# Optimization experiments

Measured on AMD Instinct MI355X. Metric: run time of the kernel, lower is better.

Reference implementation:

```python
import jax, jax.numpy as jnp
import numpy as np

B, DIM, T, H = 8, 1024, 2048, 16
HD = DIM // H  # per-head channel dim = 64


def _toeplitz(v):
    # v: (H, T) -> (H, T, T) with M[h, i, j] = v[h, j - i] if j >= i else 0
    m = v.shape[-1]
    i = jnp.arange(m)[:, None]
    j = jnp.arange(m)[None, :]
    idx = jnp.where(j >= i, j - i, 0)
    return jnp.where(j >= i, v[..., idx], jnp.zeros((), v.dtype))


def setup_inputs() -> dict:
    key = jax.random.key(0)
    ks = jax.random.split(key, 5)
    s = 1.0 / np.sqrt(DIM)
    return {
        "x": jax.random.normal(ks[0], (B, DIM, T), jnp.float32),
        "w_in": jax.random.normal(ks[1], (DIM, DIM), jnp.float32) * s,
        "b_in": jnp.zeros((DIM,), jnp.float32),
        "w_out": jax.random.normal(ks[2], (DIM, DIM), jnp.float32) * s,
        "b_out": jnp.zeros((DIM,), jnp.float32),
        "toep_w": jax.random.normal(ks[3], (H, T), jnp.float32) * 0.02,
        "toep_b": jnp.zeros((H, T), jnp.float32),
    }


def reference(x, w_in, b_in, w_out, b_out, toep_w, toep_b):
    # x: (B, DIM, T) -> (B, T, DIM)
    xt = jnp.transpose(x, (0, 2, 1))
    h1 = xt @ w_in.T + b_in  # (B, T, DIM)
    # (B, T, H*HD) -> (B, H, HD, T)
    p = jnp.transpose(h1.reshape(B, T, H, HD), (0, 2, 3, 1))
    M = _toeplitz(toep_w)  # (H, T, T)
    # bmm with per-head causal Toeplitz matrix + per-head bias over time
    conv = jnp.einsum("bhdt,htu->bhdu", p, M) + toep_b[None, :, None, :]
    # (B, H, HD, T) -> (B, T, H*HD)
    merged = jnp.transpose(conv, (0, 3, 1, 2)).reshape(B, T, DIM)
    out = merged @ w_out.T + b_out  # (B, T, DIM)
    return jnp.transpose(out, (0, 2, 1))  # (B, DIM, T)
```

## Files before the change

### kernel.cpp

```cpp
#include <hip/hip_runtime.h>
#include <hip/hip_bf16.h>
#include <stdint.h>

#define B_   8
#define DIM  1024
#define T_   2048
#define H_   16
#define HD   64

typedef __attribute__((ext_vector_type(8))) short bf16x8;
typedef __attribute__((ext_vector_type(4))) float f32x4;

__device__ __forceinline__ unsigned short f2bf(float f) {
    union { float f; unsigned u; } v{f};
    unsigned r = v.u + 0x7fffu + ((v.u >> 16) & 1u);
    return (unsigned short)(r >> 16);
}

__device__ __forceinline__ void gl_lds16(const unsigned short* g, unsigned short* l) {
    __builtin_amdgcn_global_load_lds(
        (const __attribute__((address_space(1))) void*)(const void*)g,
        (__attribute__((address_space(3))) void*)(void*)l,
        16, 0, 0);
}

__device__ __forceinline__ bf16x8 ld_frag(const unsigned short* smem, int row, int cg) {
    return *reinterpret_cast<const bf16x8*>(smem + row * 64 + (((cg) ^ (row & 7)) << 3));
}

__global__ void xpose_cast(const float* __restrict__ x, unsigned short* __restrict__ xt) {
    __shared__ float tile[64][65];
    const int b = blockIdx.z;
    const int d0 = blockIdx.y * 64, t0 = blockIdx.x * 64;
    const int tid = threadIdx.x;
    const int c = tid & 63;
    const int r0 = tid >> 6;

    const float* xp = x + ((size_t)b * DIM + d0) * T_ + t0;
#pragma unroll
    for (int i = 0; i < 16; ++i) {
        int r = r0 + i * 4;
        tile[r][c] = xp[(size_t)r * T_ + c];
    }
    __syncthreads();
    unsigned short* op = xt + ((size_t)b * T_ + t0) * DIM + d0;
#pragma unroll
    for (int i = 0; i < 16; ++i) {
        int r = r0 + i * 4;
        op[(size_t)r * DIM + c] = f2bf(tile[c][r]);
    }
}

__global__ void cast_weights(const float* __restrict__ w_in, const float* __restrict__ w_out,
                             const float* __restrict__ tw,
                             unsigned short* __restrict__ w_in_b, unsigned short* __restrict__ w_out_b,
                             unsigned short* __restrict__ tw_b) {
    int i = blockIdx.x * 256 + threadIdx.x;
    if (i < DIM * DIM) {
        w_in_b[i]  = f2bf(w_in[i]);
        w_out_b[i] = f2bf(w_out[i]);
    }
    if (i < H_ * T_) tw_b[i] = f2bf(tw[i]);
}

__global__ void gen_mfrag(const unsigned short* __restrict__ twb, unsigned short* __restrict__ Mf) {
    const int h = blockIdx.y, dg = blockIdx.x;
    const int D = (dg - 1) * 64;
    unsigned short* out = Mf + (((size_t)h * 32 + dg) << 13);
    for (int v = threadIdx.x; v < 1024; v += 256) {
        int cg = v >> 7, row = v & 127;
        bf16x8 w;
#pragma unroll
        for (int j = 0; j < 8; ++j) {
            int lag = D + row - (cg * 8 + j);
            w[j] = (lag >= 0) ? (short)twb[h * T_ + lag] : (short)0;
        }
        *reinterpret_cast<bf16x8*>(out + (size_t)v * 8) = w;
    }
}

template <bool OUT_BF16>
__global__ void gemm_k(const unsigned short* __restrict__ Aw,
                       const unsigned short* __restrict__ Bm,
                       const float* __restrict__ bias,
                       void* __restrict__ Out) {
    __shared__ __align__(16) unsigned short As[128 * 64];
    __shared__ __align__(16) unsigned short Bs[128 * 64];

    const int flat = blockIdx.x;
    const int wid  = (flat & 7) * 128 + (flat >> 3);
    const int nx   = wid & 15;
    const int my   = (wid >> 4) & 7;
    const int b    = wid >> 7;

    const int tid = threadIdx.x, lane = tid & 63, wv = tid >> 6;
    const int m0 = my * 128;
    const int n0 = nx * 128;
    const unsigned short* Bb = Bm + (size_t)b * T_ * DIM;

    const int wr = wv >> 1, wc = wv & 1;
    const int lrow = lane & 15, lg = lane >> 4;

    f32x4 acc[4][4] = {};

    for (int k0 = 0; k0 < DIM; k0 += 64) {
        __syncthreads();
#pragma unroll
        for (int it = 0; it < 4; ++it) {
            int ch = wv * 4 + it;
            int r  = ch * 8 + (lane >> 3);
            int g  = (lane & 7) ^ (lane >> 3);
            gl_lds16(Aw + (size_t)(m0 + r) * DIM + k0 + g * 8, As + ch * 512);
            gl_lds16(Bb + (size_t)(n0 + r) * DIM + k0 + g * 8, Bs + ch * 512);
        }
        __syncthreads();

#pragma unroll
        for (int kk = 0; kk < 2; ++kk) {
            bf16x8 af[4], bfr[4];
#pragma unroll
            for (int mt = 0; mt < 4; ++mt) af[mt]  = ld_frag(As, wr * 64 + mt * 16 + lrow, kk * 4 + lg);
#pragma unroll
            for (int nt = 0; nt < 4; ++nt) bfr[nt] = ld_frag(Bs, wc * 64 + nt * 16 + lrow, kk * 4 + lg);
#pragma unroll
            for (int mt = 0; mt < 4; ++mt)
#pragma unroll
                for (int nt = 0; nt < 4; ++nt)
                    acc[mt][nt] = __builtin_amdgcn_mfma_f32_16x16x32_bf16(af[mt], bfr[nt], acc[mt][nt], 0, 0, 0);
        }
    }

    const size_t ob = (size_t)b * DIM * T_;
#pragma unroll
    for (int mt = 0; mt < 4; ++mt) {
        int d = m0 + wr * 64 + mt * 16 + lg * 4;
#pragma unroll
        for (int nt = 0; nt < 4; ++nt) {
            int t = n0 + wc * 64 + nt * 16 + lrow;
#pragma unroll
            for (int r = 0; r < 4; ++r) {
                float v = acc[mt][nt][r] + bias[d + r];
                if constexpr (OUT_BF16)
                    ((unsigned short*)Out)[ob + (size_t)(d + r) * T_ + t] = f2bf(v);
                else
                    ((float*)Out)[ob + (size_t)(d + r) * T_ + t] = v;
            }
        }
    }
}

__global__ void conv4_k(const unsigned short* __restrict__ H1,
                        const unsigned short* __restrict__ Mf,
                        const float* __restrict__ tb,
                        unsigned short* __restrict__ Cb) {
    __shared__ __align__(16) unsigned short Ps[2][64 * 64];

    const int flat = blockIdx.x;
    const int wid  = (flat & 7) * 128 + (flat >> 3);
    const int bx   = wid & 7;
    const int b    = (wid >> 3) & 7;
    const int h    = wid >> 6;

    const int tid = threadIdx.x, lane = tid & 63, wv = tid >> 6;
    const unsigned short* Hb = H1 + ((size_t)b * DIM + h * HD) * T_;
    const unsigned short* Ah = Mf + ((size_t)h * 32) * 8192;

    const int lrow = lane & 15, lg = lane >> 4;
    const int rsub = lane >> 3;
    const int g = (lane & 7) ^ rsub;

    const int aoff = (lg * 128 + wv * 32 + lrow) * 8;

#pragma unroll
    for (int ph = 0; ph < 2; ++ph) {
        const int ut = ph ? bx : (T_ / 128 - 1 - bx);
        const int u0 = ut * 128;
        const int nk = 2 * ut + 2;
        f32x4 acc[2][4] = {};

#pragma unroll
        for (int it = 0; it < 2; ++it) {
            int ch = wv * 2 + it;
            int r  = ch * 8 + rsub;
            gl_lds16(Hb + (size_t)r * T_ + g * 8, &Ps[0][0] + ch * 512);
        }
        __syncthreads();

        for (int kt = 0; kt < nk; ++kt) {
            const int cur = kt & 1;
            if (kt + 1 < nk) {
                const int t0n = (kt + 1) * 64;
#pragma unroll
                for (int it = 0; it < 2; ++it) {
                    int ch = wv * 2 + it;
                    int r  = ch * 8 + rsub;
                    gl_lds16(Hb + (size_t)r * T_ + t0n + g * 8, &Ps[cur ^ 1][0] + ch * 512);
                }
            }
            const int dg = 2 * ut - kt + 1;
            const unsigned short* At = Ah + (size_t)dg * 8192;
            bf16x8 af0[2], af1[2];
#pragma unroll
            for (int mt = 0; mt < 2; ++mt) {
                af0[mt] = *reinterpret_cast<const bf16x8*>(At + aoff + mt * 128);
                af1[mt] = *reinterpret_cast<const bf16x8*>(At + 4096 + aoff + mt * 128);
            }
            const unsigned short* Pb = &Ps[cur][0];
            bf16x8 bfr[4];
#pragma unroll
            for (int nt = 0; nt < 4; ++nt) bfr[nt] = ld_frag(Pb, nt * 16 + lrow, lg);
#pragma unroll
            for (int mt = 0; mt < 2; ++mt)
#pragma unroll
                for (int nt = 0; nt < 4; ++nt)
                    acc[mt][nt] = __builtin_amdgcn_mfma_f32_16x16x32_bf16(af0[mt], bfr[nt], acc[mt][nt], 0, 0, 0);
#pragma unroll
            for (int nt = 0; nt < 4; ++nt) bfr[nt] = ld_frag(Pb, nt * 16 + lrow, 4 + lg);
#pragma unroll
            for (int mt = 0; mt < 2; ++mt)
#pragma unroll
                for (int nt = 0; nt < 4; ++nt)
                    acc[mt][nt] = __builtin_amdgcn_mfma_f32_16x16x32_bf16(af1[mt], bfr[nt], acc[mt][nt], 0, 0, 0);

            __syncthreads();
        }

        const size_t base = (size_t)b * T_ * DIM + (size_t)h * HD;
#pragma unroll
        for (int mt = 0; mt < 2; ++mt) {
            int u = u0 + wv * 32 + mt * 16 + lg * 4;
            const float* tbp = tb + h * T_ + u;
            float t0v = tbp[0], t1v = tbp[1], t2v = tbp[2], t3v = tbp[3];
#pragma unroll
            for (int nt = 0; nt < 4; ++nt) {
                int d = nt * 16 + lrow;
                size_t p = base + (size_t)u * DIM + d;
                Cb[p]           = f2bf(acc[mt][nt][0] + t0v);
                Cb[p + DIM]     = f2bf(acc[mt][nt][1] + t1v);
                Cb[p + 2 * DIM] = f2bf(acc[mt][nt][2] + t2v);
                Cb[p + 3 * DIM] = f2bf(acc[mt][nt][3] + t3v);
            }
        }
    }
}

extern "C" void kernel_launch(void* const* d_in, const int* in_sizes, int n_in,
                              void* d_out, int out_size, void* d_ws, size_t ws_size,
                              hipStream_t stream) {
    (void)in_sizes; (void)n_in; (void)out_size; (void)ws_size;
    const float* x      = (const float*)d_in[0];
    const float* w_in   = (const float*)d_in[1];
    const float* b_in   = (const float*)d_in[2];
    const float* w_out  = (const float*)d_in[3];
    const float* b_out  = (const float*)d_in[4];
    const float* toep_w = (const float*)d_in[5];
    const float* toep_b = (const float*)d_in[6];

    char* ws = (char*)d_ws;
    unsigned short* XT    = (unsigned short*)(ws);
    unsigned short* H1    = (unsigned short*)(ws + 33554432);
    unsigned short* Cbuf  = (unsigned short*)(ws + 67108864);
    unsigned short* winb  = (unsigned short*)(ws + 100663296);
    unsigned short* woutb = (unsigned short*)(ws + 102760448);
    unsigned short* twb   = (unsigned short*)(ws + 104857600);
    unsigned short* Mfrag = (unsigned short*)(ws + 104923136);

    xpose_cast<<<dim3(T_ / 64, DIM / 64, B_), dim3(256), 0, stream>>>(x, XT);
    cast_weights<<<dim3((DIM * DIM) / 256), dim3(256), 0, stream>>>(w_in, w_out, toep_w, winb, woutb, twb);
    gen_mfrag<<<dim3(32, H_), dim3(256), 0, stream>>>(twb, Mfrag);
    gemm_k<true><<<dim3(1024), dim3(256), 0, stream>>>(winb, XT, b_in, (void*)H1);
    conv4_k<<<dim3(1024), dim3(256), 0, stream>>>(H1, Mfrag, toep_b, Cbuf);
    gemm_k<false><<<dim3(1024), dim3(256), 0, stream>>>(woutb, Cbuf, b_out, d_out);
}
```

Measured before the change: 145.3 us.

## Double-buffer GEMM and conv LDS tiles with prefetch depth two

Both the projection GEMM and the Toeplitz conv kernel now keep two LDS stages in flight. They prefetch tiles two iterations ahead using explicit vmcnt waits and raw s_barrier instead of __syncthreads. Fragments are read into registers before the buffer is refilled, and the MFMA block runs at raised wave priority. The goal is to hide global-to-LDS latency behind matrix math. The cost is doubled LDS in the GEMM (64KB), which may cut occupancy, and fragile hand-tuned waitcnt logic.

```diff
diff --git a/kernel.cpp b/kernel.cpp
--- a/kernel.cpp
+++ b/kernel.cpp
@@ -84,8 +84,8 @@
                        const unsigned short* __restrict__ Bm,
                        const float* __restrict__ bias,
                        void* __restrict__ Out) {
-    __shared__ __align__(16) unsigned short As[128 * 64];
-    __shared__ __align__(16) unsigned short Bs[128 * 64];
+    __shared__ __align__(16) unsigned short As[2][128 * 64];
+    __shared__ __align__(16) unsigned short Bs[2][128 * 64];
 
     const int flat = blockIdx.x;
     const int wid  = (flat & 7) * 128 + (flat >> 3);
@@ -100,34 +100,62 @@
 
     const int wr = wv >> 1, wc = wv & 1;
     const int lrow = lane & 15, lg = lane >> 4;
+    const int rsub = lane >> 3;
+    const int g = (lane & 7) ^ rsub;
 
     f32x4 acc[4][4] = {};
 
-    for (int k0 = 0; k0 < DIM; k0 += 64) {
-        __syncthreads();
+    auto STAGE = [&](int kt, int p) {
+        const int k0 = kt * 64;
 #pragma unroll
         for (int it = 0; it < 4; ++it) {
             int ch = wv * 4 + it;
-            int r  = ch * 8 + (lane >> 3);
-            int g  = (lane & 7) ^ (lane >> 3);
-            gl_lds16(Aw + (size_t)(m0 + r) * DIM + k0 + g * 8, As + ch * 512);
-            gl_lds16(Bb + (size_t)(n0 + r) * DIM + k0 + g * 8, Bs + ch * 512);
-        }
-        __syncthreads();
-
-#pragma unroll
-        for (int kk = 0; kk < 2; ++kk) {
-            bf16x8 af[4], bfr[4];
-#pragma unroll
-            for (int mt = 0; mt < 4; ++mt) af[mt]  = ld_frag(As, wr * 64 + mt * 16 + lrow, kk * 4 + lg);
-#pragma unroll
-            for (int nt = 0; nt < 4; ++nt) bfr[nt] = ld_frag(Bs, wc * 64 + nt * 16 + lrow, kk * 4 + lg);
-#pragma unroll
-            for (int mt = 0; mt < 4; ++mt)
-#pragma unroll
-                for (int nt = 0; nt < 4; ++nt)
-                    acc[mt][nt] = __builtin_amdgcn_mfma_f32_16x16x32_bf16(af[mt], bfr[nt], acc[mt][nt], 0, 0, 0);
-        }
+            int r  = ch * 8 + rsub;
+            gl_lds16(Aw + (size_t)(m0 + r) * DIM + k0 + g * 8, &As[p][0] + ch * 512);
+            gl_lds16(Bb + (size_t)(n0 + r) * DIM + k0 + g * 8, &Bs[p][0] + ch * 512);
+        }
+    };
+
+    STAGE(0, 0);
+    STAGE(1, 1);
+
+    const int NT = DIM / 64;
+    for (int i = 0; i < NT; ++i) {
+        const int cur = i & 1;
+        if (i + 1 < NT) asm volatile("s_waitcnt vmcnt(8)" ::: "memory");
+        else            asm volatile("s_waitcnt vmcnt(0)" ::: "memory");
+        __builtin_amdgcn_s_barrier();
+        __builtin_amdgcn_sched_barrier(0);
+
+        const unsigned short* Ab = &As[cur][0];
+        const unsigned short* Bf = &Bs[cur][0];
+        bf16x8 a0[4], b0[4], a1[4], b1[4];
+#pragma unroll
+        for (int mt = 0; mt < 4; ++mt) a0[mt] = ld_frag(Ab, wr * 64 + mt * 16 + lrow, lg);
+#pragma unroll
+        for (int nt = 0; nt < 4; ++nt) b0[nt] = ld_frag(Bf, wc * 64 + nt * 16 + lrow, lg);
+#pragma unroll
+        for (int mt = 0; mt < 4; ++mt) a1[mt] = ld_frag(Ab, wr * 64 + mt * 16 + lrow, 4 + lg);
+#pragma unroll
+        for (int nt = 0; nt < 4; ++nt) b1[nt] = ld_frag(Bf, wc * 64 + nt * 16 + lrow, 4 + lg);
+
+        asm volatile("s_waitcnt lgkmcnt(0)" ::: "memory");
+        __builtin_amdgcn_s_barrier();
+        __builtin_amdgcn_sched_barrier(0);
+        if (i + 2 < NT) STAGE(i + 2, cur);
+
+        __builtin_amdgcn_s_setprio(1);
+#pragma unroll
+        for (int mt = 0; mt < 4; ++mt)
+#pragma unroll
+            for (int nt = 0; nt < 4; ++nt)
+                acc[mt][nt] = __builtin_amdgcn_mfma_f32_16x16x32_bf16(a0[mt], b0[nt], acc[mt][nt], 0, 0, 0);
+#pragma unroll
+        for (int mt = 0; mt < 4; ++mt)
+#pragma unroll
+            for (int nt = 0; nt < 4; ++nt)
+                acc[mt][nt] = __builtin_amdgcn_mfma_f32_16x16x32_bf16(a1[mt], b1[nt], acc[mt][nt], 0, 0, 0);
+        __builtin_amdgcn_s_setprio(0);
     }
 
     const size_t ob = (size_t)b * DIM * T_;
@@ -149,7 +177,7 @@
     }
 }
 
-__global__ void conv4_k(const unsigned short* __restrict__ H1,
+__global__ void conv5_k(const unsigned short* __restrict__ H1,
                         const unsigned short* __restrict__ Mf,
                         const float* __restrict__ tb,
                         unsigned short* __restrict__ Cb) {
@@ -171,6 +199,16 @@
 
     const int aoff = (lg * 128 + wv * 32 + lrow) * 8;
 
+    auto PSTAGE = [&](int kt, int p) {
+        const int t0 = kt * 64;
+#pragma unroll
+        for (int it = 0; it < 2; ++it) {
+            int ch = wv * 2 + it;
+            int r  = ch * 8 + rsub;
+            gl_lds16(Hb + (size_t)r * T_ + t0 + g * 8, &Ps[p][0] + ch * 512);
+        }
+    };
+
 #pragma unroll
     for (int ph = 0; ph < 2; ++ph) {
         const int ut = ph ? bx : (T_ / 128 - 1 - bx);
@@ -178,25 +216,23 @@
         const int nk = 2 * ut + 2;
         f32x4 acc[2][4] = {};
 
-#pragma unroll
-        for (int it = 0; it < 2; ++it) {
-            int ch = wv * 2 + it;
-            int r  = ch * 8 + rsub;
-            gl_lds16(Hb + (size_t)r * T_ + g * 8, &Ps[0][0] + ch * 512);
-        }
-        __syncthreads();
+        PSTAGE(0, 0);
+        PSTAGE(1, 1);
 
         for (int kt = 0; kt < nk; ++kt) {
             const int cur = kt & 1;
-            if (kt + 1 < nk) {
-                const int t0n = (kt + 1) * 64;
-#pragma unroll
-                for (int it = 0; it < 2; ++it) {
-                    int ch = wv * 2 + it;
-                    int r  = ch * 8 + rsub;
-                    gl_lds16(Hb + (size_t)r * T_ + t0n + g * 8, &Ps[cur ^ 1][0] + ch * 512);
-                }
-            }
+            if (kt + 1 < nk) asm volatile("s_waitcnt vmcnt(2)" ::: "memory");
+            else             asm volatile("s_waitcnt vmcnt(0)" ::: "memory");
+            __builtin_amdgcn_s_barrier();
+            __builtin_amdgcn_sched_barrier(0);
+
+            const unsigned short* Pb = &Ps[cur][0];
+            bf16x8 p0[4], p1[4];
+#pragma unroll
+            for (int nt = 0; nt < 4; ++nt) p0[nt] = ld_frag(Pb, nt * 16 + lrow, lg);
+#pragma unroll
+            for (int nt = 0; nt < 4; ++nt) p1[nt] = ld_frag(Pb, nt * 16 + lrow, 4 + lg);
+
             const int dg = 2 * ut - kt + 1;
             const unsigned short* At = Ah + (size_t)dg * 8192;
             bf16x8 af0[2], af1[2];
@@ -205,24 +241,24 @@
                 af0[mt] = *reinterpret_cast<const bf16x8*>(At + aoff + mt * 128);
                 af1[mt] = *reinterpret_cast<const bf16x8*>(At + 4096 + aoff + mt * 128);
             }
-            const unsigned short* Pb = &Ps[cur][0];
-            bf16x8 bfr[4];
-#pragma unroll
-            for (int nt = 0; nt < 4; ++nt) bfr[nt] = ld_frag(Pb, nt * 16 + lrow, lg);
+
+            asm volatile("s_waitcnt lgkmcnt(0)" ::: "memory");
+            __builtin_amdgcn_s_barrier();
+            __builtin_amdgcn_sched_barrier(0);
+            if (kt + 2 < nk) PSTAGE(kt + 2, cur);
+
+            __builtin_amdgcn_s_setprio(1);
 #pragma unroll
             for (int mt = 0; mt < 2; ++mt)
 #pragma unroll
                 for (int nt = 0; nt < 4; ++nt)
-                    acc[mt][nt] = __builtin_amdgcn_mfma_f32_16x16x32_bf16(af0[mt], bfr[nt], acc[mt][nt], 0, 0, 0);
-#pragma unroll
-            for (int nt = 0; nt < 4; ++nt) bfr[nt] = ld_frag(Pb, nt * 16 + lrow, 4 + lg);
+                    acc[mt][nt] = __builtin_amdgcn_mfma_f32_16x16x32_bf16(af0[mt], p0[nt], acc[mt][nt], 0, 0, 0);
 #pragma unroll
             for (int mt = 0; mt < 2; ++mt)
 #pragma unroll
                 for (int nt = 0; nt < 4; ++nt)
-                    acc[mt][nt] = __builtin_amdgcn_mfma_f32_16x16x32_bf16(af1[mt], bfr[nt], acc[mt][nt], 0, 0, 0);
-
-            __syncthreads();
+                    acc[mt][nt] = __builtin_amdgcn_mfma_f32_16x16x32_bf16(af1[mt], p1[nt], acc[mt][nt], 0, 0, 0);
+            __builtin_amdgcn_s_setprio(0);
         }
 
         const size_t base = (size_t)b * T_ * DIM + (size_t)h * HD;
@@ -269,6 +305,6 @@
     cast_weights<<<dim3((DIM * DIM) / 256), dim3(256), 0, stream>>>(w_in, w_out, toep_w, winb, woutb, twb);
     gen_mfrag<<<dim3(32, H_), dim3(256), 0, stream>>>(twb, Mfrag);
     gemm_k<true><<<dim3(1024), dim3(256), 0, stream>>>(winb, XT, b_in, (void*)H1);
-    conv4_k<<<dim3(1024), dim3(256), 0, stream>>>(H1, Mfrag, toep_b, Cbuf);
+    conv5_k<<<dim3(1024), dim3(256), 0, stream>>>(H1, Mfrag, toep_b, Cbuf);
     gemm_k<false><<<dim3(1024), dim3(256), 0, stream>>>(woutb, Cbuf, b_out, d_out);
 }
```

After: 319.5 us. 120% more time.

## Double-buffer GEMM LDS tiles and vectorize transpose-cast stores

Applied to the files above, without the earlier changes.

The projection GEMM kernel now keeps two LDS buffers for the A and B tiles. It issues the global-to-LDS load for the next K tile before computing on the current one, with a single barrier per iteration, so load latency can overlap the MFMAs. The transpose-cast kernel also writes four bf16 values per thread as one 8-byte store instead of scalar 2-byte stores. Doubling the GEMM's LDS footprint to 64 KB may reduce occupancy.

```diff
diff --git a/kernel.cpp b/kernel.cpp
--- a/kernel.cpp
+++ b/kernel.cpp
@@ -10,6 +10,7 @@
 
 typedef __attribute__((ext_vector_type(8))) short bf16x8;
 typedef __attribute__((ext_vector_type(4))) float f32x4;
+typedef __attribute__((ext_vector_type(4))) unsigned short u16x4;
 
 __device__ __forceinline__ unsigned short f2bf(float f) {
     union { float f; unsigned u; } v{f};
@@ -44,10 +45,15 @@
     }
     __syncthreads();
     unsigned short* op = xt + ((size_t)b * T_ + t0) * DIM + d0;
-#pragma unroll
-    for (int i = 0; i < 16; ++i) {
-        int r = r0 + i * 4;
-        op[(size_t)r * DIM + c] = f2bf(tile[c][r]);
+    const int ci = (tid & 15) * 4;
+    const int rr = tid >> 4;
+#pragma unroll
+    for (int i = 0; i < 4; ++i) {
+        int r = rr + i * 16;
+        u16x4 v;
+#pragma unroll
+        for (int j = 0; j < 4; ++j) v[j] = f2bf(tile[ci + j][r]);
+        *reinterpret_cast<u16x4*>(op + (size_t)r * DIM + ci) = v;
     }
 }
 
@@ -84,8 +90,8 @@
                        const unsigned short* __restrict__ Bm,
                        const float* __restrict__ bias,
                        void* __restrict__ Out) {
-    __shared__ __align__(16) unsigned short As[128 * 64];
-    __shared__ __align__(16) unsigned short Bs[128 * 64];
+    __shared__ __align__(16) unsigned short As[2][128 * 64];
+    __shared__ __align__(16) unsigned short Bs[2][128 * 64];
 
     const int flat = blockIdx.x;
     const int wid  = (flat & 7) * 128 + (flat >> 3);
@@ -100,34 +106,46 @@
 
     const int wr = wv >> 1, wc = wv & 1;
     const int lrow = lane & 15, lg = lane >> 4;
+    const int rsub = lane >> 3;
+    const int g = (lane & 7) ^ rsub;
 
     f32x4 acc[4][4] = {};
 
-    for (int k0 = 0; k0 < DIM; k0 += 64) {
-        __syncthreads();
+    auto STAGE = [&](int kt, int p) {
+        const int k0 = kt * 64;
 #pragma unroll
         for (int it = 0; it < 4; ++it) {
             int ch = wv * 4 + it;
-            int r  = ch * 8 + (lane >> 3);
-            int g  = (lane & 7) ^ (lane >> 3);
-            gl_lds16(Aw + (size_t)(m0 + r) * DIM + k0 + g * 8, As + ch * 512);
-            gl_lds16(Bb + (size_t)(n0 + r) * DIM + k0 + g * 8, Bs + ch * 512);
-        }
-        __syncthreads();
-
+            int r  = ch * 8 + rsub;
+            gl_lds16(Aw + (size_t)(m0 + r) * DIM + k0 + g * 8, &As[p][0] + ch * 512);
+            gl_lds16(Bb + (size_t)(n0 + r) * DIM + k0 + g * 8, &Bs[p][0] + ch * 512);
+        }
+    };
+
+    STAGE(0, 0);
+    __syncthreads();
+
+    const int NT = DIM / 64;
+    for (int i = 0; i < NT; ++i) {
+        const int cur = i & 1;
+        if (i + 1 < NT) STAGE(i + 1, cur ^ 1);
+
+        const unsigned short* Ab = &As[cur][0];
+        const unsigned short* Bf = &Bs[cur][0];
 #pragma unroll
         for (int kk = 0; kk < 2; ++kk) {
             bf16x8 af[4], bfr[4];
 #pragma unroll
-            for (int mt = 0; mt < 4; ++mt) af[mt]  = ld_frag(As, wr * 64 + mt * 16 + lrow, kk * 4 + lg);
-#pragma unroll
-            for (int nt = 0; nt < 4; ++nt) bfr[nt] = ld_frag(Bs, wc * 64 + nt * 16 + lrow, kk * 4 + lg);
+            for (int mt = 0; mt < 4; ++mt) af[mt]  = ld_frag(Ab, wr * 64 + mt * 16 + lrow, kk * 4 + lg);
+#pragma unroll
+            for (int nt = 0; nt < 4; ++nt) bfr[nt] = ld_frag(Bf, wc * 64 + nt * 16 + lrow, kk * 4 + lg);
 #pragma unroll
             for (int mt = 0; mt < 4; ++mt)
 #pragma unroll
                 for (int nt = 0; nt < 4; ++nt)
                     acc[mt][nt] = __builtin_amdgcn_mfma_f32_16x16x32_bf16(af[mt], bfr[nt], acc[mt][nt], 0, 0, 0);
         }
+        __syncthreads();
     }
 
     const size_t ob = (size_t)b * DIM * T_;
```

Result: slower. 155.1 us (+6.8%).

## Process two batches per conv block, vectorize transpose stores, fuse toeplitz cast

Applied to the files above, without the earlier changes.

The Toeplitz conv kernel now handles two batch elements per workgroup, so each Toeplitz matrix fragment loaded from global memory feeds twice as many MFMAs. The grid is halved and per-wave accumulators double. Separately, the transpose-cast kernel writes four bf16 values per store instead of one, and the toeplitz weight cast is folded into fragment generation, which removes one buffer. The extra accumulator registers and the halved grid (512 blocks) may reduce occupancy.

```diff
diff --git a/kernel.cpp b/kernel.cpp
--- a/kernel.cpp
+++ b/kernel.cpp
@@ -10,6 +10,7 @@
 
 typedef __attribute__((ext_vector_type(8))) short bf16x8;
 typedef __attribute__((ext_vector_type(4))) float f32x4;
+typedef __attribute__((ext_vector_type(4))) unsigned short u16x4;
 
 __device__ __forceinline__ unsigned short f2bf(float f) {
     union { float f; unsigned u; } v{f};
@@ -44,28 +45,31 @@
     }
     __syncthreads();
     unsigned short* op = xt + ((size_t)b * T_ + t0) * DIM + d0;
-#pragma unroll
-    for (int i = 0; i < 16; ++i) {
-        int r = r0 + i * 4;
-        op[(size_t)r * DIM + c] = f2bf(tile[c][r]);
+    const int ci = (tid & 15) * 4;
+    const int rr = tid >> 4;
+#pragma unroll
+    for (int i = 0; i < 4; ++i) {
+        int r = rr + i * 16;
+        u16x4 v;
+#pragma unroll
+        for (int j = 0; j < 4; ++j) v[j] = f2bf(tile[ci + j][r]);
+        *reinterpret_cast<u16x4*>(op + (size_t)r * DIM + ci) = v;
     }
 }
 
 __global__ void cast_weights(const float* __restrict__ w_in, const float* __restrict__ w_out,
-                             const float* __restrict__ tw,
-                             unsigned short* __restrict__ w_in_b, unsigned short* __restrict__ w_out_b,
-                             unsigned short* __restrict__ tw_b) {
+                             unsigned short* __restrict__ w_in_b, unsigned short* __restrict__ w_out_b) {
     int i = blockIdx.x * 256 + threadIdx.x;
     if (i < DIM * DIM) {
         w_in_b[i]  = f2bf(w_in[i]);
         w_out_b[i] = f2bf(w_out[i]);
     }
-    if (i < H_ * T_) tw_b[i] = f2bf(tw[i]);
-}
-
-__global__ void gen_mfrag(const unsigned short* __restrict__ twb, unsigned short* __restrict__ Mf) {
+}
+
+__global__ void gen_mfrag(const float* __restrict__ tw, unsigned short* __restrict__ Mf) {
     const int h = blockIdx.y, dg = blockIdx.x;
     const int D = (dg - 1) * 64;
+    const float* twh = tw + h * T_;
     unsigned short* out = Mf + (((size_t)h * 32 + dg) << 13);
     for (int v = threadIdx.x; v < 1024; v += 256) {
         int cg = v >> 7, row = v & 127;
@@ -73,7 +77,7 @@
 #pragma unroll
         for (int j = 0; j < 8; ++j) {
             int lag = D + row - (cg * 8 + j);
-            w[j] = (lag >= 0) ? (short)twb[h * T_ + lag] : (short)0;
+            w[j] = (lag >= 0) ? (short)f2bf(twh[lag]) : (short)0;
         }
         *reinterpret_cast<bf16x8*>(out + (size_t)v * 8) = w;
     }
@@ -149,54 +153,57 @@
     }
 }
 
-__global__ void conv4_k(const unsigned short* __restrict__ H1,
+__global__ void conv6_k(const unsigned short* __restrict__ H1,
                         const unsigned short* __restrict__ Mf,
                         const float* __restrict__ tb,
                         unsigned short* __restrict__ Cb) {
-    __shared__ __align__(16) unsigned short Ps[2][64 * 64];
+    __shared__ __align__(16) unsigned short Ps[2][128 * 64];
 
     const int flat = blockIdx.x;
-    const int wid  = (flat & 7) * 128 + (flat >> 3);
+    const int wid  = (flat & 7) * 64 + (flat >> 3);
     const int bx   = wid & 7;
-    const int b    = (wid >> 3) & 7;
-    const int h    = wid >> 6;
+    const int bp   = (wid >> 3) & 3;
+    const int h    = wid >> 5;
+    const int b0   = bp * 2;
 
     const int tid = threadIdx.x, lane = tid & 63, wv = tid >> 6;
-    const unsigned short* Hb = H1 + ((size_t)b * DIM + h * HD) * T_;
-    const unsigned short* Ah = Mf + ((size_t)h * 32) * 8192;
+    const unsigned short* Hb0 = H1 + ((size_t)b0 * DIM + h * HD) * T_;
+    const unsigned short* Hb1 = H1 + ((size_t)(b0 + 1) * DIM + h * HD) * T_;
+    const unsigned short* Ah  = Mf + ((size_t)h * 32) * 8192;
 
     const int lrow = lane & 15, lg = lane >> 4;
     const int rsub = lane >> 3;
     const int g = (lane & 7) ^ rsub;
 
     const int aoff = (lg * 128 + wv * 32 + lrow) * 8;
+
+    auto PSTAGE = [&](int kt, int p) {
+        const int t0 = kt * 64;
+#pragma unroll
+        for (int it = 0; it < 4; ++it) {
+            int ch = wv * 4 + it;
+            int r  = ch * 8 + rsub;
+            const unsigned short* src = (r < 64)
+                ? (Hb0 + (size_t)r * T_ + t0 + g * 8)
+                : (Hb1 + (size_t)(r - 64) * T_ + t0 + g * 8);
+            gl_lds16(src, &Ps[p][0] + ch * 512);
+        }
+    };
 
 #pragma unroll
     for (int ph = 0; ph < 2; ++ph) {
         const int ut = ph ? bx : (T_ / 128 - 1 - bx);
         const int u0 = ut * 128;
         const int nk = 2 * ut + 2;
-        f32x4 acc[2][4] = {};
-
-#pragma unroll
-        for (int it = 0; it < 2; ++it) {
-            int ch = wv * 2 + it;
-            int r  = ch * 8 + rsub;
-            gl_lds16(Hb + (size_t)r * T_ + g * 8, &Ps[0][0] + ch * 512);
-        }
+        f32x4 acc[2][8] = {};
+
+        PSTAGE(0, 0);
         __syncthreads();
 
         for (int kt = 0; kt < nk; ++kt) {
             const int cur = kt & 1;
-            if (kt + 1 < nk) {
-                const int t0n = (kt + 1) * 64;
-#pragma unroll
-                for (int it = 0; it < 2; ++it) {
-                    int ch = wv * 2 + it;
-                    int r  = ch * 8 + rsub;
-                    gl_lds16(Hb + (size_t)r * T_ + t0n + g * 8, &Ps[cur ^ 1][0] + ch * 512);
-                }
-            }
+            if (kt + 1 < nk) PSTAGE(kt + 1, cur ^ 1);
+
             const int dg = 2 * ut - kt + 1;
             const unsigned short* At = Ah + (size_t)dg * 8192;
             bf16x8 af0[2], af1[2];
@@ -206,35 +213,36 @@
                 af1[mt] = *reinterpret_cast<const bf16x8*>(At + 4096 + aoff + mt * 128);
             }
             const unsigned short* Pb = &Ps[cur][0];
-            bf16x8 bfr[4];
-#pragma unroll
-            for (int nt = 0; nt < 4; ++nt) bfr[nt] = ld_frag(Pb, nt * 16 + lrow, lg);
+            bf16x8 bfr[8];
+#pragma unroll
+            for (int nt = 0; nt < 8; ++nt) bfr[nt] = ld_frag(Pb, nt * 16 + lrow, lg);
 #pragma unroll
             for (int mt = 0; mt < 2; ++mt)
 #pragma unroll
-                for (int nt = 0; nt < 4; ++nt)
+                for (int nt = 0; nt < 8; ++nt)
                     acc[mt][nt] = __builtin_amdgcn_mfma_f32_16x16x32_bf16(af0[mt], bfr[nt], acc[mt][nt], 0, 0, 0);
 #pragma unroll
-            for (int nt = 0; nt < 4; ++nt) bfr[nt] = ld_frag(Pb, nt * 16 + lrow, 4 + lg);
+            for (int nt = 0; nt < 8; ++nt) bfr[nt] = ld_frag(Pb, nt * 16 + lrow, 4 + lg);
 #pragma unroll
             for (int mt = 0; mt < 2; ++mt)
 #pragma unroll
-                for (int nt = 0; nt < 4; ++nt)
+                for (int nt = 0; nt < 8; ++nt)
                     acc[mt][nt] = __builtin_amdgcn_mfma_f32_16x16x32_bf16(af1[mt], bfr[nt], acc[mt][nt], 0, 0, 0);
 
             __syncthreads();
         }
 
-        const size_t base = (size_t)b * T_ * DIM + (size_t)h * HD;
 #pragma unroll
         for (int mt = 0; mt < 2; ++mt) {
             int u = u0 + wv * 32 + mt * 16 + lg * 4;
             const float* tbp = tb + h * T_ + u;
             float t0v = tbp[0], t1v = tbp[1], t2v = tbp[2], t3v = tbp[3];
 #pragma unroll
-            for (int nt = 0; nt < 4; ++nt) {
-                int d = nt * 16 + lrow;
-                size_t p = base + (size_t)u * DIM + d;
+            for (int nt = 0; nt < 8; ++nt) {
+                int col = nt * 16 + lrow;
+                int bb  = b0 + (col >> 6);
+                int d   = col & 63;
+                size_t p = (size_t)bb * T_ * DIM + (size_t)u * DIM + (size_t)h * HD + d;
                 Cb[p]           = f2bf(acc[mt][nt][0] + t0v);
                 Cb[p + DIM]     = f2bf(acc[mt][nt][1] + t1v);
                 Cb[p + 2 * DIM] = f2bf(acc[mt][nt][2] + t2v);
@@ -262,13 +270,12 @@
     unsigned short* Cbuf  = (unsigned short*)(ws + 67108864);
     unsigned short* winb  = (unsigned short*)(ws + 100663296);
     unsigned short* woutb = (unsigned short*)(ws + 102760448);
-    unsigned short* twb   = (unsigned short*)(ws + 104857600);
-    unsigned short* Mfrag = (unsigned short*)(ws + 104923136);
+    unsigned short* Mfrag = (unsigned short*)(ws + 104857600);
 
     xpose_cast<<<dim3(T_ / 64, DIM / 64, B_), dim3(256), 0, stream>>>(x, XT);
-    cast_weights<<<dim3((DIM * DIM) / 256), dim3(256), 0, stream>>>(w_in, w_out, toep_w, winb, woutb, twb);
-    gen_mfrag<<<dim3(32, H_), dim3(256), 0, stream>>>(twb, Mfrag);
+    cast_weights<<<dim3((DIM * DIM) / 256), dim3(256), 0, stream>>>(w_in, w_out, winb, woutb);
+    gen_mfrag<<<dim3(32, H_), dim3(256), 0, stream>>>(toep_w, Mfrag);
     gemm_k<true><<<dim3(1024), dim3(256), 0, stream>>>(winb, XT, b_in, (void*)H1);
-    conv4_k<<<dim3(1024), dim3(256), 0, stream>>>(H1, Mfrag, toep_b, Cbuf);
+    conv6_k<<<dim3(512), dim3(256), 0, stream>>>(H1, Mfrag, toep_b, Cbuf);
     gemm_k<false><<<dim3(1024), dim3(256), 0, stream>>>(woutb, Cbuf, b_out, d_out);
 }
```

New measurement: 160.1 us. 10.3% more time.
